# Kernel optimization log

Measured on AMD Instinct MI355X. Metric: run time of the kernel, lower is better.

The kernel has to match this reference:

```python
import jax, jax.numpy as jnp
import numpy as np

# iRPE config: ratio=1.9, method='euc', mode='ctx', shared_head=True, skip=1, rpe_on='k'
ALPHA, BETA, GAMMA = 1.9, 3.8, 15.2  # alpha=1*ratio, beta=2*ratio, gamma=8*ratio
NUM_HEADS = 12


def _rp_bucket_euc(height, width, skip):
    """Static relative-position bucket ids (Euclidean method, piecewise index).
    Returns (skip+L, skip+L) int array and num_buckets."""
    coords = np.stack(np.meshgrid(np.arange(height), np.arange(width), indexing='ij'), -1)
    coords = coords.reshape(-1, 2).astype(np.float64)  # (L, 2)
    diff = coords[:, None, :] - coords[None, :, :]      # (L, L, 2)
    dis = np.round(np.sqrt((diff ** 2).sum(-1)))        # (L, L), nonnegative
    # piecewise_index: identity for dis<=alpha, log-spaced (rounded, clipped at beta) beyond
    log_idx = np.minimum(
        np.round(ALPHA + np.log(np.maximum(dis, 1e-9) / ALPHA) / np.log(GAMMA / ALPHA) * (BETA - ALPHA)),
        BETA).astype(np.int64)
    bucket = np.where(dis <= ALPHA, np.round(dis).astype(np.int64), log_idx)
    bucket = bucket - bucket.min()
    nb = 2 * int(BETA) + 1  # 7
    if skip > 0:
        L = height * width
        full = np.full((skip + L, skip + L), nb, dtype=np.int64)  # extra bucket for cls token
        full[skip:, skip:] = bucket
        bucket, nb = full, nb + 1  # nb = 8
    return jnp.asarray(bucket), nb


def setup_inputs() -> dict:
    key = jax.random.key(0)
    ks = jax.random.split(key, 4)
    B, N, C = 8, 1025, 768  # 32x32 patches + 1 cls token
    hd = C // NUM_HEADS
    nb = 2 * int(BETA) + 1 + 1  # 8 buckets (incl. skip bucket)
    return {
        "x": jax.random.normal(ks[0], (B, N, C), jnp.float32),
        "qkv_w": jax.random.normal(ks[1], (3 * C, C), jnp.float32) * 0.02,
        "proj_w": jax.random.normal(ks[2], (C, C), jnp.float32) * 0.02,
        "proj_b": jnp.zeros((C,), jnp.float32),
        "rpe_w": jax.random.normal(ks[3], (hd, nb), jnp.float32) * 0.02,  # shared across heads
    }


def reference(x, qkv_w, proj_w, proj_b, rpe_w):
    B, N, C = x.shape
    H = NUM_HEADS
    hd = C // H
    scale = hd ** -0.5
    n_modalities = 1
    height = int((N // n_modalities) ** 0.5)        # 32 (mask is None path)
    skip = N - n_modalities * height * height       # 1 (cls token)
    rp_bucket, _ = _rp_bucket_euc(height, height, skip)  # (N, N) int, static

    qkv = (x @ qkv_w.T).reshape(B, N, 3, H, hd).transpose(2, 0, 3, 1, 4)  # (3,B,H,N,hd)
    q, k, v = qkv[0] * scale, qkv[1], qkv[2]
    attn = jnp.einsum('bhid,bhjd->bhij', q, k)
    # contextual RPE on keys (shared head): bias[b,h,i,j] = q[b,h,i,:] @ rpe_w[:, bucket[i,j]]
    lookup = jnp.einsum('bhid,dm->bhim', q, rpe_w)                      # (B,H,N,nb)
    bias = jnp.take_along_axis(lookup, rp_bucket[None, None, :, :], axis=3)  # (B,H,N,N)
    attn = jax.nn.softmax(attn + bias, axis=-1)
    out = jnp.einsum('bhij,bhjd->bhid', attn, v)
    out = out.transpose(0, 2, 1, 3).reshape(B, N, C)
    return out @ proj_w.T + proj_b
```

## Files before the change

### kernel.cpp

```cpp
#include <hip/hip_runtime.h>
#include <math.h>

#define B_    8
#define N_    1025
#define H_    12
#define HD_   64
#define C_    768
#define BH_   (B_*H_)
#define NTOK  (B_*N_)
#define SCALE 0.125f
#define NPAD  1092
#define NPADV 1088

#define QKV_ELEMS (BH_*N_*HD_)

#define XB_OFF_B     ((size_t)0)
#define WQKV_OFF_B   (XB_OFF_B + (size_t)NTOK*C_*2)
#define WPROJ_OFF_B  (WQKV_OFF_B + (size_t)3*C_*C_*2)
#define QB_OFF_B     (WPROJ_OFF_B + (size_t)C_*C_*2)
#define KB_OFF_B     (QB_OFF_B + (size_t)QKV_ELEMS*2)
#define AOB_OFF_B    (KB_OFF_B + (size_t)QKV_ELEMS*2)
#define VT_OFF_B     (AOB_OFF_B + (size_t)QKV_ELEMS*2)
#define BUCKET_OFF_B (VT_OFF_B + (size_t)BH_*HD_*NPADV*2)

typedef __attribute__((ext_vector_type(8))) short s8bf;
typedef __attribute__((ext_vector_type(8))) unsigned short u8s;
typedef __attribute__((ext_vector_type(4))) float v4f;
typedef unsigned short ushort_t;

#define GLOAD16(gp, lp) __builtin_amdgcn_global_load_lds( \
    (const __attribute__((address_space(1))) unsigned int*)(gp), \
    (__attribute__((address_space(3))) unsigned int*)(lp), 16, 0, 0)

__device__ __forceinline__ unsigned short f2bf(float x) {
    union { float f; unsigned u; } v; v.f = x;
    unsigned r = v.u + 0x7FFFu + ((v.u >> 16) & 1u);
    return (unsigned short)(r >> 16);
}

__global__ void bucket_kernel(unsigned char* __restrict__ bucketT) {
    int tid = blockIdx.x * 256 + threadIdx.x;
    if (tid >= N_ * NPAD) return;
    unsigned ut = (unsigned)tid;
    int j = ut / (unsigned)NPAD, i = ut % (unsigned)NPAD;
    if (i >= N_) i = N_ - 1;
    int bk;
    if (i < 1 || j < 1) {
        bk = 7;
    } else {
        int pi = i - 1, pj = j - 1;
        int dy = (pi >> 5) - (pj >> 5);
        int dx = (pi & 31) - (pj & 31);
        int d2 = dy*dy + dx*dx;
        bk = (d2 == 0) ? 0 : ((d2 <= 2) ? 1 : ((d2 <= 12) ? 2 : 3));
    }
    bucketT[tid] = (unsigned char)bk;
}

__global__ __launch_bounds__(256) void cast_kernel(
        const float* __restrict__ x, const float* __restrict__ w1,
        const float* __restrict__ w2,
        ushort_t* __restrict__ xb, ushort_t* __restrict__ w1b,
        ushort_t* __restrict__ w2b) {
    const int NX = NTOK * C_ / 8, NW1 = 3 * C_ * C_ / 8, NW2 = C_ * C_ / 8;
    int g = blockIdx.x * 256 + threadIdx.x;
    const float* src; ushort_t* dst; int idx;
    if (g < NX)                 { src = x;  dst = xb;  idx = g; }
    else if (g < NX + NW1)      { src = w1; dst = w1b; idx = g - NX; }
    else if (g < NX + NW1 + NW2){ src = w2; dst = w2b; idx = g - NX - NW1; }
    else return;
    size_t off = (size_t)idx * 8;
    float4 a = *(const float4*)(src + off);
    float4 c = *(const float4*)(src + off + 4);
    __align__(16) ushort_t h[8] = {f2bf(a.x), f2bf(a.y), f2bf(a.z), f2bf(a.w),
                                   f2bf(c.x), f2bf(c.y), f2bf(c.z), f2bf(c.w)};
    *(u8s*)(dst + off) = *(u8s*)h;
}

__global__ __launch_bounds__(256, 4) void qkv_kernel(
        const ushort_t* __restrict__ xb, const ushort_t* __restrict__ wb,
        ushort_t* __restrict__ qb, ushort_t* __restrict__ kb, ushort_t* __restrict__ vt) {
    __shared__ __align__(16) ushort_t As[128*64];
    __shared__ __align__(16) ushort_t Bs[128*64];
    const int m0 = blockIdx.x * 128, c0 = blockIdx.y * 128;
    const int t = threadIdx.x;
    const int w = t >> 6, lane = t & 63, lc = lane & 15, lq = lane >> 4;
    const int wm = (w >> 1) * 64, wn = (w & 1) * 64;
    const int srow8 = w * 32 + (lane >> 3);
    const int gsw8  = (((lane & 7) ^ (lane >> 3)) & 7) * 8;

    v4f acc[4][4];
#pragma unroll
    for (int mt = 0; mt < 4; mt++)
#pragma unroll
        for (int nt = 0; nt < 4; nt++) acc[mt][nt] = (v4f){0.f, 0.f, 0.f, 0.f};

    for (int k0 = 0; k0 < C_; k0 += 64) {
        if (k0) __syncthreads();
#pragma unroll
        for (int i = 0; i < 4; i++) {
            int row = srow8 + i * 8;
            int m = m0 + row; if (m > NTOK - 1) m = NTOK - 1;
            GLOAD16(xb + (size_t)m * C_ + k0 + gsw8,           &As[(w*32 + i*8) * 64]);
            GLOAD16(wb + (size_t)(c0 + row) * C_ + k0 + gsw8,  &Bs[(w*32 + i*8) * 64]);
        }
        __syncthreads();
#pragma unroll
        for (int kk = 0; kk < 64; kk += 32) {
            s8bf af[4], bf[4];
#pragma unroll
            for (int mt = 0; mt < 4; mt++)
                af[mt] = *(s8bf*)&As[(wm + mt*16 + lc) * 64 + ((((kk>>3) + lq) ^ (lc & 7)) * 8)];
#pragma unroll
            for (int nt = 0; nt < 4; nt++)
                bf[nt] = *(s8bf*)&Bs[(wn + nt*16 + lc) * 64 + ((((kk>>3) + lq) ^ (lc & 7)) * 8)];
#pragma unroll
            for (int mt = 0; mt < 4; mt++)
#pragma unroll
                for (int nt = 0; nt < 4; nt++)
                    acc[mt][nt] = __builtin_amdgcn_mfma_f32_16x16x32_bf16(af[mt], bf[nt], acc[mt][nt], 0, 0, 0);
        }
    }

#pragma unroll
    for (int mt = 0; mt < 4; mt++) {
#pragma unroll
        for (int r = 0; r < 4; r++) {
            int m = m0 + wm + mt*16 + lq*4 + r;
            if (m >= NTOK) continue;
            unsigned um = (unsigned)m;
            int b = um / (unsigned)N_, n = um % (unsigned)N_;
#pragma unroll
            for (int nt = 0; nt < 4; nt++) {
                int c = c0 + wn + nt*16 + lc;
                int comp = c / C_, rem = c % C_;
                int h = rem >> 6, d0 = rem & 63;
                float val = acc[mt][nt][r] * ((comp == 0) ? SCALE : 1.0f);
                if (comp == 2) {
                    vt[((size_t)((b*H_ + h)*HD_ + d0))*NPADV + n] = f2bf(val);
                } else {
                    ushort_t* dst = (comp == 0) ? qb : kb;
                    dst[((size_t)((b*H_ + h)*N_ + n))*HD_ + d0] = f2bf(val);
                }
            }
        }
    }
}

#define LDT  72
#define LUTS 9

__global__ __launch_bounds__(256) void attn_kernel(
        const ushort_t* __restrict__ qb, const ushort_t* __restrict__ kb,
        const ushort_t* __restrict__ vt, const float* __restrict__ rpe,
        const unsigned char* __restrict__ bucketT, ushort_t* __restrict__ ao) {
    __shared__ __align__(16) ushort_t Ks[64*LDT];
    __shared__ __align__(16) ushort_t Vs[64*LDT];
    __shared__ __align__(16) ushort_t Ps[64*LDT];
    __shared__ float lut[64*LUTS];

    const int bh = blockIdx.x, it = blockIdx.y;
    const int b  = bh / H_, hh = bh % H_;
    const int i0 = it * 64;
    const int t  = threadIdx.x;
    const int w  = t >> 6, lane = t & 63, lc = lane & 15, lq = lane >> 4;
    const int row_w = w * 16;

    const ushort_t* qp = qb + (size_t)bh * N_ * HD_;
    const ushort_t* kp = kb + (size_t)bh * N_ * HD_;
    const ushort_t* vp = vt + (size_t)bh * HD_ * NPADV;

    {
        int row = t >> 2, d0 = (t & 3) * 16;
        int gi = i0 + row;
        u8s h0 = (u8s)0, h1 = (u8s)0;
        if (gi < N_) {
            h0 = *(const u8s*)(qp + (size_t)gi * HD_ + d0);
            h1 = *(const u8s*)(qp + (size_t)gi * HD_ + d0 + 8);
        }
        *(u8s*)&Vs[row*LDT + d0]     = h0;
        *(u8s*)&Vs[row*LDT + d0 + 8] = h1;
    }
    if (t < 64) {
        float4 r0 = *(const float4*)(rpe + t*8);
        float4 r1 = *(const float4*)(rpe + t*8 + 4);
        Ps[0*LDT + t] = f2bf(r0.x); Ps[1*LDT + t] = f2bf(r0.y);
        Ps[2*LDT + t] = f2bf(r0.z); Ps[3*LDT + t] = f2bf(r0.w);
        Ps[4*LDT + t] = f2bf(r1.x); Ps[5*LDT + t] = f2bf(r1.y);
        Ps[6*LDT + t] = f2bf(r1.z); Ps[7*LDT + t] = f2bf(r1.w);
    } else if (t < 128) {
        int idx = t - 64;
        int m = 8 + (idx >> 3), c = (idx & 7) * 8;
        *(u8s*)&Ps[m*LDT + c] = (u8s)0;
    }
    __syncthreads();

    s8bf qf0 = *(s8bf*)&Vs[(row_w + lc)*LDT + lq*8];
    s8bf qf1 = *(s8bf*)&Vs[(row_w + lc)*LDT + 32 + lq*8];

    {
        s8bf rf0 = *(s8bf*)&Ps[lc*LDT + lq*8];
        s8bf rf1 = *(s8bf*)&Ps[lc*LDT + 32 + lq*8];
        v4f la = (v4f){0.f, 0.f, 0.f, 0.f};
        la = __builtin_amdgcn_mfma_f32_16x16x32_bf16(qf0, rf0, la, 0, 0, 0);
        la = __builtin_amdgcn_mfma_f32_16x16x32_bf16(qf1, rf1, la, 0, 0, 0);
        if (lc < 8) {
#pragma unroll
            for (int r = 0; r < 4; r++)
                lut[(row_w + lq*4 + r)*LUTS + lc] = la[r];
        }
    }

    const int srow = t >> 2, sd0 = (t & 3) * 16;
    u8s krg0, krg1, vrg0, vrg1;
    {
        const ushort_t* ks = kp + (size_t)srow * HD_ + sd0;
        krg0 = *(const u8s*)ks; krg1 = *(const u8s*)(ks + 8);
        const ushort_t* vs = vp + (size_t)srow * NPADV + sd0;
        vrg0 = *(const u8s*)vs; vrg1 = *(const u8s*)(vs + 8);
    }
    const int ibase = i0 + row_w + lq*4;
    unsigned bk4[4];
#pragma unroll
    for (int t4 = 0; t4 < 4; t4++) {
        int jb = t4*16 + lc;
        bk4[t4] = *(const unsigned*)(bucketT + (size_t)jb * NPAD + ibase);
    }

    v4f o[4];
    float lsum[4];
#pragma unroll
    for (int dt = 0; dt < 4; dt++) o[dt] = (v4f){0.f, 0.f, 0.f, 0.f};
#pragma unroll
    for (int r = 0; r < 4; r++) lsum[r] = 0.f;

    for (int jt = 0; jt < 17; jt++) {
        const int j0 = jt * 64;
        __syncthreads();
        {
            ushort_t* kd = &Ks[srow*LDT + sd0];
            *(u8s*)kd = krg0; *(u8s*)(kd + 8) = krg1;
            ushort_t* vd = &Vs[srow*LDT + sd0];
            *(u8s*)vd = vrg0; *(u8s*)(vd + 8) = vrg1;
        }
        __syncthreads();

        unsigned bk4n[4];
        if (jt < 16) {
            int gj = j0 + 64 + srow; if (gj > N_ - 1) gj = N_ - 1;
            const ushort_t* ks = kp + (size_t)gj * HD_ + sd0;
            krg0 = *(const u8s*)ks; krg1 = *(const u8s*)(ks + 8);
            const ushort_t* vs = vp + (size_t)srow * NPADV + (j0 + 64) + sd0;
            vrg0 = *(const u8s*)vs; vrg1 = *(const u8s*)(vs + 8);
#pragma unroll
            for (int t4 = 0; t4 < 4; t4++) {
                int jb = j0 + 64 + t4*16 + lc; if (jb > N_ - 1) jb = N_ - 1;
                bk4n[t4] = *(const unsigned*)(bucketT + (size_t)jb * NPAD + ibase);
            }
        }

        v4f acc[4];
#pragma unroll
        for (int t4 = 0; t4 < 4; t4++) acc[t4] = (v4f){0.f, 0.f, 0.f, 0.f};
#pragma unroll
        for (int t4 = 0; t4 < 4; t4++) {
            s8bf kf0 = *(s8bf*)&Ks[(t4*16 + lc)*LDT + lq*8];
            s8bf kf1 = *(s8bf*)&Ks[(t4*16 + lc)*LDT + 32 + lq*8];
            acc[t4] = __builtin_amdgcn_mfma_f32_16x16x32_bf16(qf0, kf0, acc[t4], 0, 0, 0);
            acc[t4] = __builtin_amdgcn_mfma_f32_16x16x32_bf16(qf1, kf1, acc[t4], 0, 0, 0);
        }

#pragma unroll
        for (int t4 = 0; t4 < 4; t4++) {
#pragma unroll
            for (int r = 0; r < 4; r++) {
                int bk = (bk4[t4] >> (8*r)) & 0xFF;
                float sv = acc[t4][r] + lut[(row_w + lq*4 + r)*LUTS + bk];
                float p = __expf(sv);
                if (jt == 16 && (t4*16 + lc) > 0) p = 0.f;
                lsum[r] += p;
                Ps[(row_w + lq*4 + r)*LDT + t4*16 + lc] = f2bf(p);
            }
        }
#pragma unroll
        for (int t4 = 0; t4 < 4; t4++) bk4[t4] = bk4n[t4];

        s8bf pf0 = *(s8bf*)&Ps[(row_w + lc)*LDT + lq*8];
        s8bf pf1 = *(s8bf*)&Ps[(row_w + lc)*LDT + 32 + lq*8];
#pragma unroll
        for (int dt = 0; dt < 4; dt++) {
            s8bf vf0 = *(s8bf*)&Vs[(dt*16 + lc)*LDT + lq*8];
            s8bf vf1 = *(s8bf*)&Vs[(dt*16 + lc)*LDT + 32 + lq*8];
            o[dt] = __builtin_amdgcn_mfma_f32_16x16x32_bf16(pf0, vf0, o[dt], 0, 0, 0);
            o[dt] = __builtin_amdgcn_mfma_f32_16x16x32_bf16(pf1, vf1, o[dt], 0, 0, 0);
        }
    }

#pragma unroll
    for (int r = 0; r < 4; r++) {
        float sm = lsum[r];
        sm += __shfl_xor(sm, 1);
        sm += __shfl_xor(sm, 2);
        sm += __shfl_xor(sm, 4);
        sm += __shfl_xor(sm, 8);
        int i = i0 + row_w + lq*4 + r;
        if (i < N_) {
            float inv = 1.0f / sm;
#pragma unroll
            for (int dt = 0; dt < 4; dt++)
                ao[((size_t)(b*N_ + i))*C_ + hh*HD_ + dt*16 + lc] = f2bf(o[dt][r] * inv);
        }
    }
}

__global__ __launch_bounds__(256) void proj_kernel(
        const ushort_t* __restrict__ ab, const ushort_t* __restrict__ wb,
        const float* __restrict__ bias, float* __restrict__ out) {
    __shared__ __align__(16) ushort_t As[128*64];
    __shared__ __align__(16) ushort_t Bs[128*64];
    const int m0 = blockIdx.x * 128, c0 = blockIdx.y * 128;
    const int t = threadIdx.x;
    const int w = t >> 6, lane = t & 63, lc = lane & 15, lq = lane >> 4;
    const int wm = (w >> 1) * 64, wn = (w & 1) * 64;
    const int srow8 = w * 32 + (lane >> 3);
    const int gsw8  = (((lane & 7) ^ (lane >> 3)) & 7) * 8;

    v4f acc[4][4];
#pragma unroll
    for (int mt = 0; mt < 4; mt++)
#pragma unroll
        for (int nt = 0; nt < 4; nt++) acc[mt][nt] = (v4f){0.f, 0.f, 0.f, 0.f};

    for (int k0 = 0; k0 < C_; k0 += 64) {
        if (k0) __syncthreads();
#pragma unroll
        for (int i = 0; i < 4; i++) {
            int row = srow8 + i * 8;
            int m = m0 + row; if (m > NTOK - 1) m = NTOK - 1;
            GLOAD16(ab + (size_t)m * C_ + k0 + gsw8,           &As[(w*32 + i*8) * 64]);
            GLOAD16(wb + (size_t)(c0 + row) * C_ + k0 + gsw8,  &Bs[(w*32 + i*8) * 64]);
        }
        __syncthreads();
#pragma unroll
        for (int kk = 0; kk < 64; kk += 32) {
            s8bf af[4], bf[4];
#pragma unroll
            for (int mt = 0; mt < 4; mt++)
                af[mt] = *(s8bf*)&As[(wm + mt*16 + lc) * 64 + ((((kk>>3) + lq) ^ (lc & 7)) * 8)];
#pragma unroll
            for (int nt = 0; nt < 4; nt++)
                bf[nt] = *(s8bf*)&Bs[(wn + nt*16 + lc) * 64 + ((((kk>>3) + lq) ^ (lc & 7)) * 8)];
#pragma unroll
            for (int mt = 0; mt < 4; mt++)
#pragma unroll
                for (int nt = 0; nt < 4; nt++)
                    acc[mt][nt] = __builtin_amdgcn_mfma_f32_16x16x32_bf16(af[mt], bf[nt], acc[mt][nt], 0, 0, 0);
        }
    }

    float pb[4];
#pragma unroll
    for (int nt = 0; nt < 4; nt++) pb[nt] = bias[c0 + wn + nt*16 + lc];
#pragma unroll
    for (int mt = 0; mt < 4; mt++) {
#pragma unroll
        for (int r = 0; r < 4; r++) {
            int m = m0 + wm + mt*16 + lq*4 + r;
            if (m >= NTOK) continue;
#pragma unroll
            for (int nt = 0; nt < 4; nt++) {
                int c = c0 + wn + nt*16 + lc;
                out[(size_t)m * C_ + c] = acc[mt][nt][r] + pb[nt];
            }
        }
    }
}

extern "C" void kernel_launch(void* const* d_in, const int* in_sizes, int n_in,
                              void* d_out, int out_size, void* d_ws, size_t ws_size,
                              hipStream_t stream) {
    const float* x      = (const float*)d_in[0];
    const float* qkv_w  = (const float*)d_in[1];
    const float* proj_w = (const float*)d_in[2];
    const float* proj_b = (const float*)d_in[3];
    const float* rpe_w  = (const float*)d_in[4];
    float* out = (float*)d_out;

    char* ws = (char*)d_ws;
    ushort_t* xb   = (ushort_t*)(ws + XB_OFF_B);
    ushort_t* wqkv = (ushort_t*)(ws + WQKV_OFF_B);
    ushort_t* wprj = (ushort_t*)(ws + WPROJ_OFF_B);
    ushort_t* qb   = (ushort_t*)(ws + QB_OFF_B);
    ushort_t* kb   = (ushort_t*)(ws + KB_OFF_B);
    ushort_t* aob  = (ushort_t*)(ws + AOB_OFF_B);
    ushort_t* vt   = (ushort_t*)(ws + VT_OFF_B);
    unsigned char* bucketT = (unsigned char*)(ws + BUCKET_OFF_B);

    const int ncast = (NTOK*C_ + 3*C_*C_ + C_*C_) / 8;
    bucket_kernel<<<dim3((N_*NPAD + 255)/256), 256, 0, stream>>>(bucketT);
    cast_kernel<<<dim3((ncast + 255)/256), 256, 0, stream>>>(x, qkv_w, proj_w, xb, wqkv, wprj);
    qkv_kernel<<<dim3(65, 18), 256, 0, stream>>>(xb, wqkv, qb, kb, vt);
    attn_kernel<<<dim3(96, 17), 256, 0, stream>>>(qb, kb, vt, rpe_w, bucketT, aob);
    proj_kernel<<<dim3(65, 6), 256, 0, stream>>>(aob, wprj, proj_b, out);
}
```

Baseline: 253.6 us.

## Double-buffer LDS in QKV and projection GEMMs with async global-to-LDS prefetch

Both the QKV and output-projection GEMMs now use two LDS buffer pairs. The next K-tile is issued with global_load_lds while the current tile feeds the MFMAs, and explicit vmcnt waits plus raw s_barrier with sched barriers replace the per-step __syncthreads. The aim is to hide global-load latency behind matrix math. LDS use per block doubles to 64KB, which can cut occupancy, and the qkv kernel drops its min-blocks launch bound.

```diff
diff --git a/kernel.cpp b/kernel.cpp
--- a/kernel.cpp
+++ b/kernel.cpp
@@ -31,6 +31,12 @@
 #define GLOAD16(gp, lp) __builtin_amdgcn_global_load_lds( \
     (const __attribute__((address_space(1))) unsigned int*)(gp), \
     (__attribute__((address_space(3))) unsigned int*)(lp), 16, 0, 0)
+
+#define SBAR() do { \
+    __builtin_amdgcn_sched_barrier(0); \
+    asm volatile("s_barrier" ::: "memory"); \
+    __builtin_amdgcn_sched_barrier(0); \
+} while (0)
 
 __device__ __forceinline__ unsigned short f2bf(float x) {
     union { float f; unsigned u; } v; v.f = x;
@@ -77,11 +83,13 @@
     *(u8s*)(dst + off) = *(u8s*)h;
 }
 
-__global__ __launch_bounds__(256, 4) void qkv_kernel(
+__global__ __launch_bounds__(256) void qkv_kernel(
         const ushort_t* __restrict__ xb, const ushort_t* __restrict__ wb,
         ushort_t* __restrict__ qb, ushort_t* __restrict__ kb, ushort_t* __restrict__ vt) {
-    __shared__ __align__(16) ushort_t As[128*64];
-    __shared__ __align__(16) ushort_t Bs[128*64];
+    __shared__ __align__(16) ushort_t As0[128*64];
+    __shared__ __align__(16) ushort_t Bs0[128*64];
+    __shared__ __align__(16) ushort_t As1[128*64];
+    __shared__ __align__(16) ushort_t Bs1[128*64];
     const int m0 = blockIdx.x * 128, c0 = blockIdx.y * 128;
     const int t = threadIdx.x;
     const int w = t >> 6, lane = t & 63, lc = lane & 15, lq = lane >> 4;
@@ -95,31 +103,55 @@
 #pragma unroll
         for (int nt = 0; nt < 4; nt++) acc[mt][nt] = (v4f){0.f, 0.f, 0.f, 0.f};
 
-    for (int k0 = 0; k0 < C_; k0 += 64) {
-        if (k0) __syncthreads();
+    auto STAGE = [&](ushort_t* Ad, ushort_t* Bd, int k0) {
 #pragma unroll
         for (int i = 0; i < 4; i++) {
             int row = srow8 + i * 8;
             int m = m0 + row; if (m > NTOK - 1) m = NTOK - 1;
-            GLOAD16(xb + (size_t)m * C_ + k0 + gsw8,           &As[(w*32 + i*8) * 64]);
-            GLOAD16(wb + (size_t)(c0 + row) * C_ + k0 + gsw8,  &Bs[(w*32 + i*8) * 64]);
-        }
-        __syncthreads();
+            GLOAD16(xb + (size_t)m * C_ + k0 + gsw8,           &Ad[(w*32 + i*8) * 64]);
+            GLOAD16(wb + (size_t)(c0 + row) * C_ + k0 + gsw8,  &Bd[(w*32 + i*8) * 64]);
+        }
+    };
+    auto COMPUTE = [&](const ushort_t* A, const ushort_t* B) {
 #pragma unroll
         for (int kk = 0; kk < 64; kk += 32) {
             s8bf af[4], bf[4];
 #pragma unroll
             for (int mt = 0; mt < 4; mt++)
-                af[mt] = *(s8bf*)&As[(wm + mt*16 + lc) * 64 + ((((kk>>3) + lq) ^ (lc & 7)) * 8)];
+                af[mt] = *(const s8bf*)&A[(wm + mt*16 + lc) * 64 + ((((kk>>3) + lq) ^ (lc & 7)) * 8)];
 #pragma unroll
             for (int nt = 0; nt < 4; nt++)
-                bf[nt] = *(s8bf*)&Bs[(wn + nt*16 + lc) * 64 + ((((kk>>3) + lq) ^ (lc & 7)) * 8)];
+                bf[nt] = *(const s8bf*)&B[(wn + nt*16 + lc) * 64 + ((((kk>>3) + lq) ^ (lc & 7)) * 8)];
 #pragma unroll
             for (int mt = 0; mt < 4; mt++)
 #pragma unroll
                 for (int nt = 0; nt < 4; nt++)
                     acc[mt][nt] = __builtin_amdgcn_mfma_f32_16x16x32_bf16(af[mt], bf[nt], acc[mt][nt], 0, 0, 0);
         }
+    };
+
+    STAGE(As0, Bs0, 0);
+#pragma unroll
+    for (int it = 0; it < 6; ++it) {
+        const int k0 = it * 128;
+        if (k0 + 64 < C_) {
+            STAGE(As1, Bs1, k0 + 64);
+            asm volatile("s_waitcnt vmcnt(8)" ::: "memory");
+        } else {
+            asm volatile("s_waitcnt vmcnt(0)" ::: "memory");
+        }
+        SBAR();
+        COMPUTE(As0, Bs0);
+        SBAR();
+        if (k0 + 128 < C_) {
+            STAGE(As0, Bs0, k0 + 128);
+            asm volatile("s_waitcnt vmcnt(8)" ::: "memory");
+        } else {
+            asm volatile("s_waitcnt vmcnt(0)" ::: "memory");
+        }
+        SBAR();
+        COMPUTE(As1, Bs1);
+        if (it < 5) SBAR();
     }
 
 #pragma unroll
@@ -316,8 +348,10 @@
 __global__ __launch_bounds__(256) void proj_kernel(
         const ushort_t* __restrict__ ab, const ushort_t* __restrict__ wb,
         const float* __restrict__ bias, float* __restrict__ out) {
-    __shared__ __align__(16) ushort_t As[128*64];
-    __shared__ __align__(16) ushort_t Bs[128*64];
+    __shared__ __align__(16) ushort_t As0[128*64];
+    __shared__ __align__(16) ushort_t Bs0[128*64];
+    __shared__ __align__(16) ushort_t As1[128*64];
+    __shared__ __align__(16) ushort_t Bs1[128*64];
     const int m0 = blockIdx.x * 128, c0 = blockIdx.y * 128;
     const int t = threadIdx.x;
     const int w = t >> 6, lane = t & 63, lc = lane & 15, lq = lane >> 4;
@@ -331,31 +365,55 @@
 #pragma unroll
         for (int nt = 0; nt < 4; nt++) acc[mt][nt] = (v4f){0.f, 0.f, 0.f, 0.f};
 
-    for (int k0 = 0; k0 < C_; k0 += 64) {
-        if (k0) __syncthreads();
+    auto STAGE = [&](ushort_t* Ad, ushort_t* Bd, int k0) {
 #pragma unroll
         for (int i = 0; i < 4; i++) {
             int row = srow8 + i * 8;
             int m = m0 + row; if (m > NTOK - 1) m = NTOK - 1;
-            GLOAD16(ab + (size_t)m * C_ + k0 + gsw8,           &As[(w*32 + i*8) * 64]);
-            GLOAD16(wb + (size_t)(c0 + row) * C_ + k0 + gsw8,  &Bs[(w*32 + i*8) * 64]);
-        }
-        __syncthreads();
+            GLOAD16(ab + (size_t)m * C_ + k0 + gsw8,           &Ad[(w*32 + i*8) * 64]);
+            GLOAD16(wb + (size_t)(c0 + row) * C_ + k0 + gsw8,  &Bd[(w*32 + i*8) * 64]);
+        }
+    };
+    auto COMPUTE = [&](const ushort_t* A, const ushort_t* B) {
 #pragma unroll
         for (int kk = 0; kk < 64; kk += 32) {
             s8bf af[4], bf[4];
 #pragma unroll
             for (int mt = 0; mt < 4; mt++)
-                af[mt] = *(s8bf*)&As[(wm + mt*16 + lc) * 64 + ((((kk>>3) + lq) ^ (lc & 7)) * 8)];
+                af[mt] = *(const s8bf*)&A[(wm + mt*16 + lc) * 64 + ((((kk>>3) + lq) ^ (lc & 7)) * 8)];
 #pragma unroll
             for (int nt = 0; nt < 4; nt++)
-                bf[nt] = *(s8bf*)&Bs[(wn + nt*16 + lc) * 64 + ((((kk>>3) + lq) ^ (lc & 7)) * 8)];
+                bf[nt] = *(const s8bf*)&B[(wn + nt*16 + lc) * 64 + ((((kk>>3) + lq) ^ (lc & 7)) * 8)];
 #pragma unroll
             for (int mt = 0; mt < 4; mt++)
 #pragma unroll
                 for (int nt = 0; nt < 4; nt++)
                     acc[mt][nt] = __builtin_amdgcn_mfma_f32_16x16x32_bf16(af[mt], bf[nt], acc[mt][nt], 0, 0, 0);
         }
+    };
+
+    STAGE(As0, Bs0, 0);
+#pragma unroll
+    for (int it = 0; it < 6; ++it) {
+        const int k0 = it * 128;
+        if (k0 + 64 < C_) {
+            STAGE(As1, Bs1, k0 + 64);
+            asm volatile("s_waitcnt vmcnt(8)" ::: "memory");
+        } else {
+            asm volatile("s_waitcnt vmcnt(0)" ::: "memory");
+        }
+        SBAR();
+        COMPUTE(As0, Bs0);
+        SBAR();
+        if (k0 + 128 < C_) {
+            STAGE(As0, Bs0, k0 + 128);
+            asm volatile("s_waitcnt vmcnt(8)" ::: "memory");
+        } else {
+            asm volatile("s_waitcnt vmcnt(0)" ::: "memory");
+        }
+        SBAR();
+        COMPUTE(As1, Bs1);
+        if (it < 5) SBAR();
     }
 
     float pb[4];
```

Result: slower. 259.4 us (+2.3%).
